# Performance work log

Hardware: AMD Instinct MI355X
Metric: run time of the kernel (lower is better)

The kernel has to match this reference:

```python
import jax, jax.numpy as jnp
import numpy as np

DIM = 2048
NUM_HEADS = 16
HEAD_DIM = DIM // NUM_HEADS
ROPE_BASE = 10000.0


def _rope_cache(seq_len):
    inv_freq = 1.0 / (ROPE_BASE ** (jnp.arange(0, HEAD_DIM, 2, dtype=jnp.float32) / HEAD_DIM))
    t = jnp.arange(seq_len, dtype=jnp.float32)
    freqs = jnp.einsum('i,j->ij', t, inv_freq)          # [S, HEAD_DIM//2]
    emb = jnp.concatenate([freqs, freqs], axis=-1)       # [S, HEAD_DIM]
    return jnp.cos(emb), jnp.sin(emb)


def _rotate_half(x):
    x1, x2 = jnp.split(x, 2, axis=-1)
    return jnp.concatenate([-x2, x1], axis=-1)


def setup_inputs() -> dict:
    key = jax.random.key(0)
    kx, kq, ko = jax.random.split(key, 3)
    B, S = 2, 2048
    x = jax.random.normal(kx, (B, S, DIM), dtype=jnp.float32)
    # torch nn.Linear(dim, 3*dim) weight has shape [3*dim, dim]; y = x @ W.T
    w_qkv = jax.random.normal(kq, (3 * DIM, DIM), dtype=jnp.float32) * (DIM ** -0.5)
    w_out = jax.random.normal(ko, (DIM, DIM), dtype=jnp.float32) * (DIM ** -0.5)
    return {"x": x, "w_qkv": w_qkv, "w_out": w_out}


def reference(x, w_qkv, w_out):
    B, S, _ = x.shape
    qkv = x @ w_qkv.T                                   # [B, S, 3*DIM]
    q, k, v = jnp.split(qkv, 3, axis=-1)
    def to_heads(t):
        return t.reshape(B, S, NUM_HEADS, HEAD_DIM).transpose(0, 2, 1, 3)  # [B, H, S, d]
    q, k, v = to_heads(q), to_heads(k), to_heads(v)

    cos, sin = _rope_cache(S)                           # [S, d]
    cos = cos[None, None, :, :]
    sin = sin[None, None, :, :]
    q = q * cos + _rotate_half(q) * sin
    k = k * cos + _rotate_half(k) * sin

    scale = HEAD_DIM ** -0.5
    scores = jnp.einsum('bhqd,bhkd->bhqk', q, k) * scale  # [B, H, S, S]
    causal = jnp.tril(jnp.ones((S, S), dtype=bool))
    scores = jnp.where(causal[None, None], scores, -jnp.inf)
    attn = jax.nn.softmax(scores, axis=-1)
    out = jnp.einsum('bhqk,bhkd->bhqd', attn, v)          # [B, H, S, d]
    out = out.transpose(0, 2, 1, 3).reshape(B, S, DIM)
    return out @ w_out.T
```

## Files before the change

kernel.cpp:

```cpp
#include <hip/hip_runtime.h>
#include <cstdint>
#include <cstddef>

#define NHEADS 16
#define HDIM   128
#define BATCH  2
#define SEQ    2048
#define DMODEL 2048
#define MTOT   (BATCH*SEQ)
#define NQKV   (3*DMODEL)

typedef __attribute__((ext_vector_type(8))) __bf16 bf16x8;
typedef __attribute__((ext_vector_type(4))) float f32x4;
typedef __attribute__((ext_vector_type(8))) unsigned short ushort8v;

__device__ __forceinline__ unsigned short f2bf(float f){
  __bf16 h = (__bf16)f;
  return __builtin_bit_cast(unsigned short, h);
}
__device__ __forceinline__ float bf2f(unsigned short s){
  return __uint_as_float(((uint32_t)s) << 16);
}
__device__ __forceinline__ void gload_lds16(const void* src, void* lds_base){
  __builtin_amdgcn_global_load_lds((const __attribute__((address_space(1))) unsigned int*)src,
                                   (__attribute__((address_space(3))) unsigned int*)lds_base,
                                   16, 0, 0);
}

template<int CTRL>
__device__ __forceinline__ float dppmv(float x){
  return __uint_as_float((unsigned)__builtin_amdgcn_update_dpp(
      0, (int)__float_as_uint(x), CTRL, 0xF, 0xF, true));
}
__device__ __forceinline__ float rmax16(float x){
  x = fmaxf(x, dppmv<0x128>(x));
  x = fmaxf(x, dppmv<0x124>(x));
  x = fmaxf(x, dppmv<0x122>(x));
  x = fmaxf(x, dppmv<0x121>(x));
  return x;
}
__device__ __forceinline__ float rsum16(float x){
  x += dppmv<0x128>(x);
  x += dppmv<0x124>(x);
  x += dppmv<0x122>(x);
  x += dppmv<0x121>(x);
  return x;
}

__global__ void cast3_kernel(const float* __restrict__ s0, unsigned short* __restrict__ d0, int n0,
                             const float* __restrict__ s1, unsigned short* __restrict__ d1, int n1,
                             const float* __restrict__ s2, unsigned short* __restrict__ d2, int n2){
  const int stride = gridDim.x*blockDim.x*8;
  const int base = (blockIdx.x*blockDim.x + threadIdx.x)*8;
  #pragma unroll 1
  for (int a = 0; a < 3; ++a){
    const float* s = a==0 ? s0 : (a==1 ? s1 : s2);
    unsigned short* d = a==0 ? d0 : (a==1 ? d1 : d2);
    const int n = a==0 ? n0 : (a==1 ? n1 : n2);
    for (int i = base; i < n; i += stride){
      float4 x = *reinterpret_cast<const float4*>(s + i);
      float4 y = *reinterpret_cast<const float4*>(s + i + 4);
      ushort8v o;
      o[0]=f2bf(x.x); o[1]=f2bf(x.y); o[2]=f2bf(x.z); o[3]=f2bf(x.w);
      o[4]=f2bf(y.x); o[5]=f2bf(y.y); o[6]=f2bf(y.z); o[7]=f2bf(y.w);
      *reinterpret_cast<ushort8v*>(d + i) = o;
    }
  }
}

template<int MODE>
__global__ __launch_bounds__(512, 2) void gemm2(
    const unsigned short* __restrict__ A,
    const unsigned short* __restrict__ Bw,
    float* __restrict__ Cf,
    unsigned short* __restrict__ qo,
    unsigned short* __restrict__ ko,
    unsigned short* __restrict__ vo,
    int M, int N, int K)
{
  __shared__ __align__(16) unsigned short smem[49152];
  auto lds = reinterpret_cast<unsigned short (*)[3][128*64]>(smem);

  const int lane = threadIdx.x & 63;
  const int wid  = threadIdx.x >> 6;
  const int wm = wid >> 2, wn = wid & 3;
  const int hi = lane >> 4;
  const int l15 = lane & 15;

  const int nwg = gridDim.x * gridDim.y;
  const int bid = blockIdx.y * gridDim.x + blockIdx.x;
  const int swz = (bid & 7) * (nwg >> 3) + (bid >> 3);
  const int by = swz & 31;
  const int bx = swz >> 5;
  const int m0 = by * 128;
  const int n0 = bx * 256;

  const int NT = K >> 6;

  auto stage = [&](const unsigned short* base, int row0, int k0, int buf, int slot){
    const int rlo = wid << 4;
    #pragma unroll
    for (int i=0;i<2;++i){
      const int r = rlo + i*8 + (lane>>3);
      const int csrc = ((lane&7) ^ (lane>>3)) << 3;
      gload_lds16(base + (size_t)(row0 + r)*K + k0 + csrc,
                  &lds[buf][slot][(rlo + i*8)*64]);
    }
  };
  auto frag = [&](const unsigned short* h, int r, int s){
    return *reinterpret_cast<const bf16x8*>(h + r*64 + ((s ^ (r&7)) << 3));
  };

  f32x4 acc[4][4];
  #pragma unroll
  for (int i=0;i<4;++i)
    #pragma unroll
    for (int j=0;j<4;++j) acc[i][j] = (f32x4){0.f,0.f,0.f,0.f};

  stage(A,  m0,      0, 0, 0);
  stage(Bw, n0,      0, 0, 1);
  stage(Bw, n0+128,  0, 0, 2);
  if (NT > 1){
    stage(A, m0, 64, 1, 0);
    asm volatile("s_waitcnt vmcnt(2)" ::: "memory");
  } else {
    asm volatile("s_waitcnt vmcnt(0)" ::: "memory");
  }
  __builtin_amdgcn_sched_barrier(0);
  __builtin_amdgcn_s_barrier();

  bf16x8 Ar[4][2];
  bf16x8 Br[2][2];

  auto tile_body = [&](int kt, int cur){
    const int nxt = cur ^ 1;
    const unsigned short* Ah = &lds[cur][0][0];
    const unsigned short* Bh = &lds[cur][1 + (wn>>1)][0];
    const int rbase = (wn & 1) * 64;

    #pragma unroll
    for (int fm=0;fm<4;++fm)
      #pragma unroll
      for (int kk=0;kk<2;++kk)
        Ar[fm][kk] = frag(Ah, wm*64 + fm*16 + l15, kk*4 + hi);
    #pragma unroll
    for (int nf=0;nf<2;++nf)
      #pragma unroll
      for (int kk=0;kk<2;++kk)
        Br[nf][kk] = frag(Bh, rbase + nf*16 + l15, kk*4 + hi);
    if (kt+1 < NT){
      stage(Bw, n0,     (kt+1)*64, nxt, 1);
      stage(Bw, n0+128, (kt+1)*64, nxt, 2);
    }
    asm volatile("s_waitcnt lgkmcnt(8)" ::: "memory");
    __builtin_amdgcn_sched_barrier(0);
    __builtin_amdgcn_s_barrier();
    asm volatile("s_waitcnt lgkmcnt(0)" ::: "memory");
    __builtin_amdgcn_sched_barrier(0);
    __builtin_amdgcn_s_setprio(1);
    #pragma unroll
    for (int fm=0;fm<4;++fm){
      acc[fm][0] = __builtin_amdgcn_mfma_f32_16x16x32_bf16(Ar[fm][0], Br[0][0], acc[fm][0], 0,0,0);
      acc[fm][0] = __builtin_amdgcn_mfma_f32_16x16x32_bf16(Ar[fm][1], Br[0][1], acc[fm][0], 0,0,0);
      acc[fm][1] = __builtin_amdgcn_mfma_f32_16x16x32_bf16(Ar[fm][0], Br[1][0], acc[fm][1], 0,0,0);
      acc[fm][1] = __builtin_amdgcn_mfma_f32_16x16x32_bf16(Ar[fm][1], Br[1][1], acc[fm][1], 0,0,0);
    }
    __builtin_amdgcn_s_setprio(0);
    __builtin_amdgcn_sched_barrier(0);
    __builtin_amdgcn_s_barrier();

    #pragma unroll
    for (int nf=0;nf<2;++nf)
      #pragma unroll
      for (int kk=0;kk<2;++kk)
        Br[nf][kk] = frag(Bh, rbase + 32 + nf*16 + l15, kk*4 + hi);
    if (kt+2 < NT) stage(A, m0, (kt+2)*64, cur, 0);
    __builtin_amdgcn_sched_barrier(0);
    __builtin_amdgcn_s_barrier();
    asm volatile("s_waitcnt lgkmcnt(0)" ::: "memory");
    __builtin_amdgcn_sched_barrier(0);
    __builtin_amdgcn_s_setprio(1);
    #pragma unroll
    for (int fm=0;fm<4;++fm){
      acc[fm][2] = __builtin_amdgcn_mfma_f32_16x16x32_bf16(Ar[fm][0], Br[0][0], acc[fm][2], 0,0,0);
      acc[fm][2] = __builtin_amdgcn_mfma_f32_16x16x32_bf16(Ar[fm][1], Br[0][1], acc[fm][2], 0,0,0);
      acc[fm][3] = __builtin_amdgcn_mfma_f32_16x16x32_bf16(Ar[fm][0], Br[1][0], acc[fm][3], 0,0,0);
      acc[fm][3] = __builtin_amdgcn_mfma_f32_16x16x32_bf16(Ar[fm][1], Br[1][1], acc[fm][3], 0,0,0);
    }
    __builtin_amdgcn_s_setprio(0);
    if (kt+2 < NT)      asm volatile("s_waitcnt vmcnt(2)" ::: "memory");
    else if (kt+1 < NT) asm volatile("s_waitcnt vmcnt(0)" ::: "memory");
    __builtin_amdgcn_sched_barrier(0);
    __builtin_amdgcn_s_barrier();
  };

  for (int kt2 = 0; kt2 < NT; kt2 += 2){
    tile_body(kt2,     0);
    tile_body(kt2 + 1, 1);
  }

  if (MODE == 0 && (n0 >> 11) == 2){
    __builtin_amdgcn_s_barrier();
    unsigned short* trsp = smem;
    #pragma unroll
    for (int fm=0;fm<4;++fm){
      const int srow = wm*64 + fm*16 + hi*4;
      #pragma unroll
      for (int p=0;p<4;++p){
        const int dcol = wn*64 + p*16 + l15;
        f32x4 v = acc[fm][p];
        ushort4 pk;
        pk.x=f2bf(v[0]); pk.y=f2bf(v[1]); pk.z=f2bf(v[2]); pk.w=f2bf(v[3]);
        *reinterpret_cast<ushort4*>(trsp + dcol*136 + srow) = pk;
      }
    }
    __syncthreads();
    const int bb  = m0 >> 11;
    const int ss0 = m0 & 2047;
    const size_t vrow = (size_t)(bb*2048 + (n0 - 4096));
    const int t = threadIdx.x;
    #pragma unroll
    for (int it=0; it<8; ++it){
      const int dl = it*32 + (t>>4);
      const int ch = t & 15;
      ushort8v val = *reinterpret_cast<const ushort8v*>(trsp + dl*136 + ch*8);
      *reinterpret_cast<ushort8v*>(vo + (vrow + dl)*SEQ + ss0 + ch*8) = val;
    }
  } else {
    #pragma unroll
    for (int fm=0;fm<4;++fm){
      const int row0 = m0 + wm*64 + fm*16 + (hi<<2);
      #pragma unroll
      for (int p=0;p<4;++p){
        const int col = n0 + wn*64 + p*16 + l15;
        f32x4 v = acc[fm][p];
        if (MODE == 1){
          #pragma unroll
          for (int r=0;r<4;++r) Cf[(size_t)(row0+r)*N + col] = v[r];
        } else {
          const int part = col >> 11;
          const int hh = (col >> 7) & 15;
          const int d  = col & 127;
          const int bb = row0 >> 11;
          const int ss = row0 & 2047;
          unsigned short* base = (part == 0 ? qo : ko)
                               + ((size_t)(bb*NHEADS+hh)*SEQ + ss)*HDIM + d;
          #pragma unroll
          for (int r=0;r<4;++r) base[r*HDIM] = f2bf(v[r]);
        }
      }
    }
  }
}

__global__ void rope_kernel(unsigned short* __restrict__ qh, unsigned short* __restrict__ kh){
  const int idx = blockIdx.x * blockDim.x + threadIdx.x;
  const int j  = idx & 63;
  const int s  = (idx >> 6) & 2047;
  const int bh = (idx >> 17) & 31;
  const int t  = idx >> 22;
  unsigned short* base = (t ? kh : qh) + ((size_t)bh*SEQ + s)*HDIM;
  const float x1 = bf2f(base[j]);
  const float x2 = bf2f(base[j+64]);
  const float inv = exp2f(-(float)j * (13.287712379549449f/64.f));
  const float ang = (float)s * inv;
  float sn, cs;
  sincosf(ang, &sn, &cs);
  float o1 = x1*cs - x2*sn;
  float o2 = x2*cs + x1*sn;
  const float QSCALE = 0.08838834764831845f * 1.4426950408889634f;
  if (t == 0){ o1 *= QSCALE; o2 *= QSCALE; }
  base[j]    = f2bf(o1);
  base[j+64] = f2bf(o2);
}

__global__ __launch_bounds__(256, 1) void attn_kernel(
    const unsigned short* __restrict__ qh,
    const unsigned short* __restrict__ kh,
    const unsigned short* __restrict__ vT,
    unsigned short* __restrict__ ao)
{
  __shared__ __align__(16) unsigned short Ks[2][64*128];
  __shared__ __align__(16) unsigned short Vs[2][128*64];
  __shared__ __align__(16) unsigned short Ps[4][32*64];

  const int lane = threadIdx.x & 63;
  const int wid  = threadIdx.x >> 6;
  const int hi   = lane >> 4;
  const int l15  = lane & 15;
  const int pr = blockIdx.x;
  const int bh = blockIdx.y;
  const int b_ = bh >> 4, h_ = bh & 15;

  const unsigned short* Qb = qh + (size_t)bh * SEQ * HDIM;
  const unsigned short* Kb = kh + (size_t)bh * SEQ * HDIM;
  const unsigned short* Vb = vT + (size_t)bh * HDIM * SEQ;

  auto stageKV = [&](int kg, int buf){
    #pragma unroll
    for (int i=0;i<4;++i){
      const int r  = (wid*4+i)*4 + (lane>>4);
      const int cb = ((lane&15)<<4) ^ ((r&7)<<4);
      gload_lds16(Kb + (size_t)(kg*64 + r)*HDIM + (cb>>1), &Ks[buf][0] + (wid*4+i)*512);
    }
    #pragma unroll
    for (int i=0;i<4;++i){
      const int d  = (wid*4+i)*8 + (lane>>3);
      const int cb = ((lane&7)<<4) ^ ((d&7)<<4);
      gload_lds16(Vb + (size_t)d*SEQ + kg*64 + (cb>>1), &Vs[buf][0] + (wid*4+i)*512);
    }
  };

  for (int ph = 0; ph < 2; ++ph){
    const int qt = ph ? (15 - pr) : pr;
    const int qrow0w = qt*128 + wid*32;

    bf16x8 qf[2][4];
    #pragma unroll
    for (int fi=0; fi<2; ++fi){
      const int qr = qrow0w + fi*16 + l15;
      #pragma unroll
      for (int ks = 0; ks < 4; ++ks)
        qf[fi][ks] = *reinterpret_cast<const bf16x8*>(Qb + (size_t)qr*HDIM + ks*32 + hi*8);
    }

    f32x4 oacc[2][8];
    #pragma unroll
    for (int fi=0;fi<2;++fi)
      #pragma unroll
      for (int t=0;t<8;++t) oacc[fi][t] = (f32x4){0.f,0.f,0.f,0.f};
    float mrun[2][4], lrun[2][4];
    #pragma unroll
    for (int fi=0;fi<2;++fi)
      #pragma unroll
      for (int r=0;r<4;++r){ mrun[fi][r] = -3.0e38f; lrun[fi][r] = 0.f; }

    const int nkt = 2*qt + 2;

    stageKV(0, 0);
    __syncthreads();

    for (int kt = 0; kt < nkt; ++kt){
      const int cur = kt & 1;
      if (kt + 1 < nkt) stageKV(kt + 1, cur ^ 1);

      if (kt*64 <= qrow0w + 31){
        f32x4 sacc[2][4];
        #pragma unroll
        for (int fi=0;fi<2;++fi)
          #pragma unroll
          for (int nt=0;nt<4;++nt) sacc[fi][nt] = (f32x4){0.f,0.f,0.f,0.f};
        __builtin_amdgcn_s_setprio(1);
        #pragma unroll
        for (int nt=0;nt<4;++nt){
          const int krow = nt*16 + l15;
          bf16x8 kf[4];
          #pragma unroll
          for (int ks=0;ks<4;++ks){
            const int cb = (ks*64 + (hi<<4)) ^ ((krow&7)<<4);
            kf[ks] = *reinterpret_cast<const bf16x8*>(&Ks[cur][0] + krow*128 + (cb>>1));
          }
          #pragma unroll
          for (int fi=0;fi<2;++fi)
            #pragma unroll
            for (int ks=0;ks<4;++ks)
              sacc[fi][nt] = __builtin_amdgcn_mfma_f32_16x16x32_bf16(qf[fi][ks], kf[ks], sacc[fi][nt], 0,0,0);
        }
        __builtin_amdgcn_s_setprio(0);

        #pragma unroll
        for (int fi=0;fi<2;++fi){
          if (kt*64 + 63 > qrow0w + fi*16){
            #pragma unroll
            for (int nt=0;nt<4;++nt){
              const int key = kt*64 + nt*16 + l15;
              #pragma unroll
              for (int r=0;r<4;++r){
                const int qr = qrow0w + fi*16 + hi*4 + r;
                if (key > qr) sacc[fi][nt][r] = -1.0e30f;
              }
            }
          }
        }

        char* pb = (char*)&Ps[wid][0];
        #pragma unroll
        for (int fi=0;fi<2;++fi){
          float fac[4];
          #pragma unroll
          for (int r=0;r<4;++r){
            float mx = fmaxf(fmaxf(sacc[fi][0][r], sacc[fi][1][r]),
                             fmaxf(sacc[fi][2][r], sacc[fi][3][r]));
            mx = rmax16(mx);
            const float mnew = fmaxf(mrun[fi][r], mx);
            fac[r] = exp2f(mrun[fi][r] - mnew);
            mrun[fi][r] = mnew;
            float ps = 0.f;
            #pragma unroll
            for (int nt=0;nt<4;++nt){
              const float p = exp2f(sacc[fi][nt][r] - mnew);
              sacc[fi][nt][r] = p;
              ps += p;
            }
            ps = rsum16(ps);
            lrun[fi][r] = lrun[fi][r]*fac[r] + ps;
          }
          #pragma unroll
          for (int t=0;t<8;++t)
            #pragma unroll
            for (int r=0;r<4;++r) oacc[fi][t][r] *= fac[r];
          #pragma unroll
          for (int nt=0;nt<4;++nt){
            const int keyb = (nt*16 + l15) << 1;
            #pragma unroll
            for (int r=0;r<4;++r){
              const int prow = fi*16 + hi*4 + r;
              *(unsigned short*)(pb + prow*128 + (keyb ^ ((prow&7)<<4))) = f2bf(sacc[fi][nt][r]);
            }
          }
        }
        asm volatile("s_waitcnt lgkmcnt(0)" ::: "memory");
        __builtin_amdgcn_sched_barrier(0);

        bf16x8 pa[2][2];
        #pragma unroll
        for (int fi=0;fi<2;++fi){
          const int prow = fi*16 + l15;
          #pragma unroll
          for (int ks=0;ks<2;++ks){
            const int pcb = (ks*64 + (hi<<4)) ^ ((prow&7)<<4);
            pa[fi][ks] = *reinterpret_cast<const bf16x8*>(pb + prow*128 + pcb);
          }
        }
        __builtin_amdgcn_s_setprio(1);
        #pragma unroll
        for (int ks=0;ks<2;++ks){
          #pragma unroll
          for (int t=0;t<8;++t){
            const int drow = t*16 + l15;
            const int vcb = (ks*64 + (hi<<4)) ^ ((drow&7)<<4);
            bf16x8 vb = *reinterpret_cast<const bf16x8*>(&Vs[cur][0] + drow*64 + (vcb>>1));
            #pragma unroll
            for (int fi=0;fi<2;++fi)
              oacc[fi][t] = __builtin_amdgcn_mfma_f32_16x16x32_bf16(pa[fi][ks], vb, oacc[fi][t], 0,0,0);
          }
        }
        __builtin_amdgcn_s_setprio(0);
      }

      __syncthreads();
    }

    #pragma unroll
    for (int fi=0;fi<2;++fi){
      float linv[4];
      #pragma unroll
      for (int r=0;r<4;++r) linv[r] = 1.0f / lrun[fi][r];
      #pragma unroll
      for (int t=0;t<8;++t){
        const int col = h_*HDIM + t*16 + l15;
        #pragma unroll
        for (int r=0;r<4;++r){
          const int s_ = qrow0w + fi*16 + hi*4 + r;
          ao[(size_t)(b_*SEQ + s_)*DMODEL + col] = f2bf(oacc[fi][t][r] * linv[r]);
        }
      }
    }
  }
}

extern "C" void kernel_launch(void* const* d_in, const int* in_sizes, int n_in,
                              void* d_out, int out_size, void* d_ws, size_t ws_size,
                              hipStream_t stream)
{
  const float* x     = (const float*)d_in[0];
  const float* w_qkv = (const float*)d_in[1];
  const float* w_out = (const float*)d_in[2];
  float* out = (float*)d_out;

  unsigned short* xb    = (unsigned short*)d_ws;
  unsigned short* wqkvb = xb    + (size_t)MTOT*DMODEL;
  unsigned short* woutb = wqkvb + (size_t)NQKV*DMODEL;
  unsigned short* qhb   = woutb + (size_t)DMODEL*DMODEL;
  unsigned short* khb   = qhb   + (size_t)MTOT*DMODEL;
  unsigned short* vtb   = khb   + (size_t)MTOT*DMODEL;
  unsigned short* aob   = vtb   + (size_t)MTOT*DMODEL;

  hipLaunchKernelGGL(cast3_kernel, dim3(1024), dim3(256), 0, stream,
                     x, xb, MTOT*DMODEL, w_qkv, wqkvb, NQKV*DMODEL, w_out, woutb, DMODEL*DMODEL);
  hipLaunchKernelGGL((gemm2<0>), dim3(NQKV/256, MTOT/128), dim3(512), 0, stream,
                     xb, wqkvb, (float*)nullptr, qhb, khb, vtb, MTOT, NQKV, DMODEL);
  hipLaunchKernelGGL(rope_kernel, dim3((2*BATCH*NHEADS*SEQ*64)/256), dim3(256), 0, stream, qhb, khb);
  hipLaunchKernelGGL(attn_kernel, dim3(8, BATCH*NHEADS), dim3(256), 0, stream, qhb, khb, vtb, aob);
  hipLaunchKernelGGL((gemm2<1>), dim3(DMODEL/256, MTOT/128), dim3(512), 0, stream,
                     aob, woutb, out, (unsigned short*)nullptr, (unsigned short*)nullptr,
                     (unsigned short*)nullptr, MTOT, DMODEL, DMODEL);
}
```

Before: 296.7 us.

## Pair low and high query tiles per block in one shared KV sweep

Each attention block now handles two 64-row query tiles, a low one and its mirrored high one, inside a single KV loop. The low tile's MFMAs and softmax are skipped once past its causal limit, so both tiles share the K/V staging. The grid doubles to 16x32 blocks and launch bounds allow two blocks per CU, aiming for better load balance and occupancy. This costs extra predicated branching and possible register pressure under the tighter occupancy bound.

New measurement: 262.6 us. 1.13x faster.

```diff
diff --git a/kernel.cpp b/kernel.cpp
--- a/kernel.cpp
+++ b/kernel.cpp
@@ -274,7 +274,7 @@
   base[j+64] = f2bf(o2);
 }
 
-__global__ __launch_bounds__(256, 1) void attn_kernel(
+__global__ __launch_bounds__(256, 2) void attn_kernel(
     const unsigned short* __restrict__ qh,
     const unsigned short* __restrict__ kh,
     const unsigned short* __restrict__ vT,
@@ -282,7 +282,7 @@
 {
   __shared__ __align__(16) unsigned short Ks[2][64*128];
   __shared__ __align__(16) unsigned short Vs[2][128*64];
-  __shared__ __align__(16) unsigned short Ps[4][32*64];
+  __shared__ __align__(16) unsigned short Ps[4][16*64];
 
   const int lane = threadIdx.x & 63;
   const int wid  = threadIdx.x >> 6;
@@ -296,6 +296,8 @@
   const unsigned short* Kb = kh + (size_t)bh * SEQ * HDIM;
   const unsigned short* Vb = vT + (size_t)bh * HDIM * SEQ;
 
+  const int qrowf[2] = { pr*64 + wid*16, (31-pr)*64 + wid*16 };
+
   auto stageKV = [&](int kg, int buf){
     #pragma unroll
     for (int i=0;i<4;++i){
@@ -311,159 +313,154 @@
     }
   };
 
-  for (int ph = 0; ph < 2; ++ph){
-    const int qt = ph ? (15 - pr) : pr;
-    const int qrow0w = qt*128 + wid*32;
-
-    bf16x8 qf[2][4];
+  bf16x8 qf[2][4];
+  #pragma unroll
+  for (int fi=0; fi<2; ++fi){
+    const int qr = qrowf[fi] + l15;
+    #pragma unroll
+    for (int ks = 0; ks < 4; ++ks)
+      qf[fi][ks] = *reinterpret_cast<const bf16x8*>(Qb + (size_t)qr*HDIM + ks*32 + hi*8);
+  }
+
+  f32x4 oacc[2][8];
+  #pragma unroll
+  for (int fi=0;fi<2;++fi)
+    #pragma unroll
+    for (int t=0;t<8;++t) oacc[fi][t] = (f32x4){0.f,0.f,0.f,0.f};
+  float mrun[2][4], lrun[2][4];
+  #pragma unroll
+  for (int fi=0;fi<2;++fi)
+    #pragma unroll
+    for (int r=0;r<4;++r){ mrun[fi][r] = -3.0e38f; lrun[fi][r] = 0.f; }
+
+  const int nkt = 32 - pr;
+
+  stageKV(0, 0);
+  __syncthreads();
+
+  for (int kt = 0; kt < nkt; ++kt){
+    const int cur = kt & 1;
+    if (kt + 1 < nkt) stageKV(kt + 1, cur ^ 1);
+
+    const bool lo_act = (kt <= pr);
+
+    f32x4 sacc[2][4];
+    #pragma unroll
+    for (int fi=0;fi<2;++fi)
+      #pragma unroll
+      for (int nt=0;nt<4;++nt) sacc[fi][nt] = (f32x4){0.f,0.f,0.f,0.f};
+    __builtin_amdgcn_s_setprio(1);
+    #pragma unroll
+    for (int nt=0;nt<4;++nt){
+      const int krow = nt*16 + l15;
+      bf16x8 kf[4];
+      #pragma unroll
+      for (int ks=0;ks<4;++ks){
+        const int cb = (ks*64 + (hi<<4)) ^ ((krow&7)<<4);
+        kf[ks] = *reinterpret_cast<const bf16x8*>(&Ks[cur][0] + krow*128 + (cb>>1));
+      }
+      #pragma unroll
+      for (int ks=0;ks<4;++ks)
+        sacc[1][nt] = __builtin_amdgcn_mfma_f32_16x16x32_bf16(qf[1][ks], kf[ks], sacc[1][nt], 0,0,0);
+      if (lo_act){
+        #pragma unroll
+        for (int ks=0;ks<4;++ks)
+          sacc[0][nt] = __builtin_amdgcn_mfma_f32_16x16x32_bf16(qf[0][ks], kf[ks], sacc[0][nt], 0,0,0);
+      }
+    }
+    __builtin_amdgcn_s_setprio(0);
+
+    char* pb = (char*)&Ps[wid][0];
     #pragma unroll
     for (int fi=0; fi<2; ++fi){
-      const int qr = qrow0w + fi*16 + l15;
-      #pragma unroll
-      for (int ks = 0; ks < 4; ++ks)
-        qf[fi][ks] = *reinterpret_cast<const bf16x8*>(Qb + (size_t)qr*HDIM + ks*32 + hi*8);
-    }
-
-    f32x4 oacc[2][8];
-    #pragma unroll
-    for (int fi=0;fi<2;++fi)
-      #pragma unroll
-      for (int t=0;t<8;++t) oacc[fi][t] = (f32x4){0.f,0.f,0.f,0.f};
-    float mrun[2][4], lrun[2][4];
-    #pragma unroll
-    for (int fi=0;fi<2;++fi)
-      #pragma unroll
-      for (int r=0;r<4;++r){ mrun[fi][r] = -3.0e38f; lrun[fi][r] = 0.f; }
-
-    const int nkt = 2*qt + 2;
-
-    stageKV(0, 0);
-    __syncthreads();
-
-    for (int kt = 0; kt < nkt; ++kt){
-      const int cur = kt & 1;
-      if (kt + 1 < nkt) stageKV(kt + 1, cur ^ 1);
-
-      if (kt*64 <= qrow0w + 31){
-        f32x4 sacc[2][4];
-        #pragma unroll
-        for (int fi=0;fi<2;++fi)
-          #pragma unroll
-          for (int nt=0;nt<4;++nt) sacc[fi][nt] = (f32x4){0.f,0.f,0.f,0.f};
-        __builtin_amdgcn_s_setprio(1);
+      if (fi == 0 && !lo_act) continue;
+
+      if (kt*64 + 63 > qrowf[fi]){
         #pragma unroll
         for (int nt=0;nt<4;++nt){
-          const int krow = nt*16 + l15;
-          bf16x8 kf[4];
-          #pragma unroll
-          for (int ks=0;ks<4;++ks){
-            const int cb = (ks*64 + (hi<<4)) ^ ((krow&7)<<4);
-            kf[ks] = *reinterpret_cast<const bf16x8*>(&Ks[cur][0] + krow*128 + (cb>>1));
-          }
-          #pragma unroll
-          for (int fi=0;fi<2;++fi)
-            #pragma unroll
-            for (int ks=0;ks<4;++ks)
-              sacc[fi][nt] = __builtin_amdgcn_mfma_f32_16x16x32_bf16(qf[fi][ks], kf[ks], sacc[fi][nt], 0,0,0);
-        }
-        __builtin_amdgcn_s_setprio(0);
-
-        #pragma unroll
-        for (int fi=0;fi<2;++fi){
-          if (kt*64 + 63 > qrow0w + fi*16){
-            #pragma unroll
-            for (int nt=0;nt<4;++nt){
-              const int key = kt*64 + nt*16 + l15;
-              #pragma unroll
-              for (int r=0;r<4;++r){
-                const int qr = qrow0w + fi*16 + hi*4 + r;
-                if (key > qr) sacc[fi][nt][r] = -1.0e30f;
-              }
-            }
-          }
-        }
-
-        char* pb = (char*)&Ps[wid][0];
-        #pragma unroll
-        for (int fi=0;fi<2;++fi){
-          float fac[4];
+          const int key = kt*64 + nt*16 + l15;
           #pragma unroll
           for (int r=0;r<4;++r){
-            float mx = fmaxf(fmaxf(sacc[fi][0][r], sacc[fi][1][r]),
-                             fmaxf(sacc[fi][2][r], sacc[fi][3][r]));
-            mx = rmax16(mx);
-            const float mnew = fmaxf(mrun[fi][r], mx);
-            fac[r] = exp2f(mrun[fi][r] - mnew);
-            mrun[fi][r] = mnew;
-            float ps = 0.f;
-            #pragma unroll
-            for (int nt=0;nt<4;++nt){
-              const float p = exp2f(sacc[fi][nt][r] - mnew);
-              sacc[fi][nt][r] = p;
-              ps += p;
-            }
-            ps = rsum16(ps);
-            lrun[fi][r] = lrun[fi][r]*fac[r] + ps;
+            const int qr = qrowf[fi] + hi*4 + r;
+            if (key > qr) sacc[fi][nt][r] = -1.0e30f;
           }
-          #pragma unroll
-          for (int t=0;t<8;++t)
-            #pragma unroll
-            for (int r=0;r<4;++r) oacc[fi][t][r] *= fac[r];
-          #pragma unroll
-          for (int nt=0;nt<4;++nt){
-            const int keyb = (nt*16 + l15) << 1;
-            #pragma unroll
-            for (int r=0;r<4;++r){
-              const int prow = fi*16 + hi*4 + r;
-              *(unsigned short*)(pb + prow*128 + (keyb ^ ((prow&7)<<4))) = f2bf(sacc[fi][nt][r]);
-            }
-          }
-        }
-        asm volatile("s_waitcnt lgkmcnt(0)" ::: "memory");
-        __builtin_amdgcn_sched_barrier(0);
-
-        bf16x8 pa[2][2];
-        #pragma unroll
-        for (int fi=0;fi<2;++fi){
-          const int prow = fi*16 + l15;
-          #pragma unroll
-          for (int ks=0;ks<2;++ks){
-            const int pcb = (ks*64 + (hi<<4)) ^ ((prow&7)<<4);
-            pa[fi][ks] = *reinterpret_cast<const bf16x8*>(pb + prow*128 + pcb);
-          }
-        }
-        __builtin_amdgcn_s_setprio(1);
+        }
+      }
+
+      float fac[4];
+      #pragma unroll
+      for (int r=0;r<4;++r){
+        float mx = fmaxf(fmaxf(sacc[fi][0][r], sacc[fi][1][r]),
+                         fmaxf(sacc[fi][2][r], sacc[fi][3][r]));
+        mx = rmax16(mx);
+        const float mnew = fmaxf(mrun[fi][r], mx);
+        fac[r] = exp2f(mrun[fi][r] - mnew);
+        mrun[fi][r] = mnew;
+        float ps = 0.f;
+        #pragma unroll
+        for (int nt=0;nt<4;++nt){
+          const float p = exp2f(sacc[fi][nt][r] - mnew);
+          sacc[fi][nt][r] = p;
+          ps += p;
+        }
+        ps = rsum16(ps);
+        lrun[fi][r] = lrun[fi][r]*fac[r] + ps;
+      }
+      #pragma unroll
+      for (int t=0;t<8;++t)
+        #pragma unroll
+        for (int r=0;r<4;++r) oacc[fi][t][r] *= fac[r];
+
+      #pragma unroll
+      for (int nt=0;nt<4;++nt){
+        const int keyb = (nt*16 + l15) << 1;
+        #pragma unroll
+        for (int r=0;r<4;++r){
+          const int prow = hi*4 + r;
+          *(unsigned short*)(pb + prow*128 + (keyb ^ ((prow&7)<<4))) = f2bf(sacc[fi][nt][r]);
+        }
+      }
+      asm volatile("s_waitcnt lgkmcnt(0)" ::: "memory");
+      __builtin_amdgcn_sched_barrier(0);
+
+      bf16x8 pa[2];
+      {
+        const int prow = l15;
         #pragma unroll
         for (int ks=0;ks<2;++ks){
-          #pragma unroll
-          for (int t=0;t<8;++t){
-            const int drow = t*16 + l15;
-            const int vcb = (ks*64 + (hi<<4)) ^ ((drow&7)<<4);
-            bf16x8 vb = *reinterpret_cast<const bf16x8*>(&Vs[cur][0] + drow*64 + (vcb>>1));
-            #pragma unroll
-            for (int fi=0;fi<2;++fi)
-              oacc[fi][t] = __builtin_amdgcn_mfma_f32_16x16x32_bf16(pa[fi][ks], vb, oacc[fi][t], 0,0,0);
-          }
-        }
-        __builtin_amdgcn_s_setprio(0);
-      }
-
-      __syncthreads();
-    }
-
-    #pragma unroll
-    for (int fi=0;fi<2;++fi){
-      float linv[4];
-      #pragma unroll
-      for (int r=0;r<4;++r) linv[r] = 1.0f / lrun[fi][r];
-      #pragma unroll
-      for (int t=0;t<8;++t){
-        const int col = h_*HDIM + t*16 + l15;
-        #pragma unroll
-        for (int r=0;r<4;++r){
-          const int s_ = qrow0w + fi*16 + hi*4 + r;
-          ao[(size_t)(b_*SEQ + s_)*DMODEL + col] = f2bf(oacc[fi][t][r] * linv[r]);
-        }
+          const int pcb = (ks*64 + (hi<<4)) ^ ((prow&7)<<4);
+          pa[ks] = *reinterpret_cast<const bf16x8*>(pb + prow*128 + pcb);
+        }
+      }
+      __builtin_amdgcn_s_setprio(1);
+      #pragma unroll
+      for (int ks=0;ks<2;++ks){
+        #pragma unroll
+        for (int t=0;t<8;++t){
+          const int drow = t*16 + l15;
+          const int vcb = (ks*64 + (hi<<4)) ^ ((drow&7)<<4);
+          bf16x8 vb = *reinterpret_cast<const bf16x8*>(&Vs[cur][0] + drow*64 + (vcb>>1));
+          oacc[fi][t] = __builtin_amdgcn_mfma_f32_16x16x32_bf16(pa[ks], vb, oacc[fi][t], 0,0,0);
+        }
+      }
+      __builtin_amdgcn_s_setprio(0);
+    }
+
+    __syncthreads();
+  }
+
+  #pragma unroll
+  for (int fi=0;fi<2;++fi){
+    float linv[4];
+    #pragma unroll
+    for (int r=0;r<4;++r) linv[r] = 1.0f / lrun[fi][r];
+    #pragma unroll
+    for (int t=0;t<8;++t){
+      const int col = h_*HDIM + t*16 + l15;
+      #pragma unroll
+      for (int r=0;r<4;++r){
+        const int s_ = qrowf[fi] + hi*4 + r;
+        ao[(size_t)(b_*SEQ + s_)*DMODEL + col] = f2bf(oacc[fi][t][r] * linv[r]);
       }
     }
   }
@@ -491,7 +488,7 @@
   hipLaunchKernelGGL((gemm2<0>), dim3(NQKV/256, MTOT/128), dim3(512), 0, stream,
                      xb, wqkvb, (float*)nullptr, qhb, khb, vtb, MTOT, NQKV, DMODEL);
   hipLaunchKernelGGL(rope_kernel, dim3((2*BATCH*NHEADS*SEQ*64)/256), dim3(256), 0, stream, qhb, khb);
-  hipLaunchKernelGGL(attn_kernel, dim3(8, BATCH*NHEADS), dim3(256), 0, stream, qhb, khb, vtb, aob);
+  hipLaunchKernelGGL(attn_kernel, dim3(16, BATCH*NHEADS), dim3(256), 0, stream, qhb, khb, vtb, aob);
   hipLaunchKernelGGL((gemm2<1>), dim3(DMODEL/256, MTOT/128), dim3(512), 0, stream,
                      aob, woutb, out, (unsigned short*)nullptr, (unsigned short*)nullptr,
                      (unsigned short*)nullptr, MTOT, DMODEL, DMODEL);
```
